# Performance work log

Hardware: AMD Instinct MI355X
Metric: run time of the kernel (lower is better)

The kernel has to match this reference:

```python
import jax, jax.numpy as jnp
import numpy as np

B, N, K = 16, 4096, 1024   # batch, mux_in, mux_out
TEMP = 2.0
COMPRESSION = 4.0


def setup_inputs() -> dict:
    key = jax.random.key(0)
    kx, kn, kl = jax.random.split(key, 3)
    x = jax.random.normal(kx, (B, N), dtype=jnp.float32)
    # Gumbel(0,1) noise, one sample per (batch, input-element), broadcast over K
    u = jax.random.uniform(kn, (B, N), dtype=jnp.float32, minval=1e-20, maxval=1.0)
    noise = -jnp.log(-jnp.log(u))
    logits = jax.random.normal(kl, (N,), dtype=jnp.float32) / COMPRESSION
    return {"x": x, "logits": logits, "noise": noise}


def reference(x, logits, noise):
    base = logits[None, :] + noise                      # [B, N] perturbed logits (same across k)
    _, topk_idx = jax.lax.top_k(base, K)                # [B, K]
    b_idx = jnp.arange(B)[:, None]

    # pos[b, i] = rank of element i in the top-k (K if not selected)
    pos = jnp.full((B, N), K, dtype=jnp.int32)
    pos = pos.at[b_idx, topk_idx].set(jnp.arange(K, dtype=jnp.int32))

    hard = jnp.zeros((B, N), dtype=base.dtype).at[b_idx, topk_idx].set(1.0)

    # Element selected at rank j is masked (-inf) for all later columns c > j.
    # Equivalent to the original scatter(-inf) -> cumsum -> re-zero sequence.
    counter = jnp.arange(K, dtype=jnp.int32)            # [K]
    masked = jnp.where(counter[None, None, :] > pos[:, :, None],
                       -jnp.inf, base[:, :, None])      # [B, N, K]

    soft = jax.nn.softmax(masked / TEMP, axis=1)        # softmax over mux_in
    collapsed = soft.sum(axis=2)                        # [B, N]

    # straight-through: hard forward, soft backward
    sample = hard - jax.lax.stop_gradient(collapsed) + collapsed
    return sample * x
```

## Files before the change

kernel.cpp:

```cpp
#include <hip/hip_runtime.h>

#define BB 16
#define NN 4096
#define KK 1024
#define THREADS 1024
#define PT (NN / THREADS)
#define NWAVES (THREADS / 64)

__device__ __forceinline__ unsigned fkey(float f) {
    unsigned u = __float_as_uint(f);
    return (u & 0x80000000u) ? ~u : (u | 0x80000000u);
}

__global__ __launch_bounds__(THREADS) void gumbel_topk_mask(
    const float* __restrict__ x,
    const float* __restrict__ logits,
    const float* __restrict__ noise,
    float* __restrict__ out)
{
    __shared__ unsigned keys[NN];
    __shared__ int wsum[NWAVES];
    __shared__ int ibcast;
    __shared__ int ecnt[THREADS];
    __shared__ int epfx[THREADS];

    const int b    = blockIdx.x;
    const int t    = threadIdx.x;
    const int lane = t & 63;
    const int wid  = t >> 6;
    const size_t row = (size_t)b * NN;

    for (int i = t; i < NN; i += THREADS)
        keys[i] = fkey(logits[i] + noise[row + i]);
    __syncthreads();

    unsigned pfx = 0u;
    for (int bit = 31; bit >= 0; --bit) {
        unsigned cand = pfx | (1u << bit);
        int cnt = 0;
        #pragma unroll
        for (int j = 0; j < PT; ++j)
            cnt += (keys[t + j * THREADS] >= cand) ? 1 : 0;
        #pragma unroll
        for (int off = 32; off > 0; off >>= 1)
            cnt += __shfl_down(cnt, off, 64);
        if (lane == 0) wsum[wid] = cnt;
        __syncthreads();
        if (t == 0) {
            int s = 0;
            for (int w = 0; w < NWAVES; ++w) s += wsum[w];
            ibcast = s;
        }
        __syncthreads();
        if (ibcast >= KK) pfx = cand;
    }
    const unsigned T = pfx;

    int packed = 0;
    #pragma unroll
    for (int j = 0; j < PT; ++j) {
        unsigned k = keys[t + j * THREADS];
        packed += (k > T) ? 1 : 0;
        packed += (k == T) ? (1 << 16) : 0;
    }
    #pragma unroll
    for (int off = 32; off > 0; off >>= 1)
        packed += __shfl_down(packed, off, 64);
    if (lane == 0) wsum[wid] = packed;
    __syncthreads();
    if (t == 0) {
        int s = 0;
        for (int w = 0; w < NWAVES; ++w) s += wsum[w];
        ibcast = s;
    }
    __syncthreads();
    const int total_g = ibcast & 0xFFFF;
    const int total_e = ibcast >> 16;
    const int rem = KK - total_g;

    const bool need_rank = (rem < total_e);
    if (need_rank) {
        int c = 0;
        for (int j = 0; j < PT; ++j)
            c += (keys[t * PT + j] == T) ? 1 : 0;
        ecnt[t] = c;
        __syncthreads();
        if (t == 0) {
            int s = 0;
            for (int i = 0; i < THREADS; ++i) { epfx[i] = s; s += ecnt[i]; }
        }
        __syncthreads();
    }

    for (int j = 0; j < PT; ++j) {
        int n = t + j * THREADS;
        unsigned k = keys[n];
        bool sel = (k > T);
        if (!sel && k == T) {
            if (!need_rank) {
                sel = true;
            } else {
                int c = n / PT;
                int r = epfx[c];
                for (int m = c * PT; m < n; ++m) r += (keys[m] == T) ? 1 : 0;
                sel = (r < rem);
            }
        }
        out[row + n] = sel ? x[row + n] : 0.0f;
    }
}

extern "C" void kernel_launch(void* const* d_in, const int* in_sizes, int n_in,
                              void* d_out, int out_size, void* d_ws, size_t ws_size,
                              hipStream_t stream) {
    const float* x      = (const float*)d_in[0];
    const float* logits = (const float*)d_in[1];
    const float* noise  = (const float*)d_in[2];
    float* out = (float*)d_out;
    (void)in_sizes; (void)n_in; (void)out_size; (void)d_ws; (void)ws_size;
    gumbel_topk_mask<<<BB, THREADS, 0, stream>>>(x, logits, noise, out);
}
```

Baseline: 25.78 us.

## Run top-k threshold search in a single wave with register keys and ballots

Replaces the 1024-thread block with one 64-lane wave per batch row, keeping 64 keys per thread in registers. The radix threshold search counts with ballot/popcount instead of shared-memory reductions and block barriers, and exits early when the count hits K exactly. Tie ranking uses a wave prefix scan, and loads and stores are vectorised. Parallelism per row drops sharply and per-thread memory accesses become strided across lanes.

```diff
diff --git a/kernel.cpp b/kernel.cpp
--- a/kernel.cpp
+++ b/kernel.cpp
@@ -3,110 +3,87 @@
 #define BB 16
 #define NN 4096
 #define KK 1024
-#define THREADS 1024
-#define PT (NN / THREADS)
-#define NWAVES (THREADS / 64)
+#define PT 64
 
 __device__ __forceinline__ unsigned fkey(float f) {
     unsigned u = __float_as_uint(f);
     return (u & 0x80000000u) ? ~u : (u | 0x80000000u);
 }
 
-__global__ __launch_bounds__(THREADS) void gumbel_topk_mask(
+__global__ __launch_bounds__(64) void gumbel_topk_mask(
     const float* __restrict__ x,
     const float* __restrict__ logits,
     const float* __restrict__ noise,
     float* __restrict__ out)
 {
-    __shared__ unsigned keys[NN];
-    __shared__ int wsum[NWAVES];
-    __shared__ int ibcast;
-    __shared__ int ecnt[THREADS];
-    __shared__ int epfx[THREADS];
+    const int b = blockIdx.x;
+    const int t = threadIdx.x;
+    const size_t row = (size_t)b * NN;
+    const int n0 = t * PT;
 
-    const int b    = blockIdx.x;
-    const int t    = threadIdx.x;
-    const int lane = t & 63;
-    const int wid  = t >> 6;
-    const size_t row = (size_t)b * NN;
-
-    for (int i = t; i < NN; i += THREADS)
-        keys[i] = fkey(logits[i] + noise[row + i]);
-    __syncthreads();
+    unsigned key[PT];
+    {
+        const float4* lg4 = (const float4*)(logits + n0);
+        const float4* nz4 = (const float4*)(noise + row + n0);
+        #pragma unroll
+        for (int q = 0; q < PT / 4; ++q) {
+            float4 l = lg4[q], z = nz4[q];
+            key[4*q+0] = fkey(l.x + z.x);
+            key[4*q+1] = fkey(l.y + z.y);
+            key[4*q+2] = fkey(l.z + z.z);
+            key[4*q+3] = fkey(l.w + z.w);
+        }
+    }
 
     unsigned pfx = 0u;
+    #pragma unroll 1
     for (int bit = 31; bit >= 0; --bit) {
-        unsigned cand = pfx | (1u << bit);
+        const unsigned cand = pfx | (1u << bit);
         int cnt = 0;
         #pragma unroll
         for (int j = 0; j < PT; ++j)
-            cnt += (keys[t + j * THREADS] >= cand) ? 1 : 0;
-        #pragma unroll
-        for (int off = 32; off > 0; off >>= 1)
-            cnt += __shfl_down(cnt, off, 64);
-        if (lane == 0) wsum[wid] = cnt;
-        __syncthreads();
-        if (t == 0) {
-            int s = 0;
-            for (int w = 0; w < NWAVES; ++w) s += wsum[w];
-            ibcast = s;
+            cnt += __popcll(__ballot(key[j] >= cand));
+        if (cnt >= KK) {
+            pfx = cand;
+            if (cnt == KK) break;
         }
-        __syncthreads();
-        if (ibcast >= KK) pfx = cand;
     }
     const unsigned T = pfx;
 
-    int packed = 0;
+    int cnt_gt = 0;
+    int ecnt   = 0;
     #pragma unroll
     for (int j = 0; j < PT; ++j) {
-        unsigned k = keys[t + j * THREADS];
-        packed += (k > T) ? 1 : 0;
-        packed += (k == T) ? (1 << 16) : 0;
+        cnt_gt += __popcll(__ballot(key[j] > T));
+        ecnt   += (key[j] == T) ? 1 : 0;
     }
+    const int rem = KK - cnt_gt;
+
+    int inc = ecnt;
     #pragma unroll
-    for (int off = 32; off > 0; off >>= 1)
-        packed += __shfl_down(packed, off, 64);
-    if (lane == 0) wsum[wid] = packed;
-    __syncthreads();
-    if (t == 0) {
-        int s = 0;
-        for (int w = 0; w < NWAVES; ++w) s += wsum[w];
-        ibcast = s;
+    for (int off = 1; off < 64; off <<= 1) {
+        int v = __shfl_up(inc, off, 64);
+        if (t >= off) inc += v;
     }
-    __syncthreads();
-    const int total_g = ibcast & 0xFFFF;
-    const int total_e = ibcast >> 16;
-    const int rem = KK - total_g;
+    int r = inc - ecnt;
 
-    const bool need_rank = (rem < total_e);
-    if (need_rank) {
-        int c = 0;
-        for (int j = 0; j < PT; ++j)
-            c += (keys[t * PT + j] == T) ? 1 : 0;
-        ecnt[t] = c;
-        __syncthreads();
-        if (t == 0) {
-            int s = 0;
-            for (int i = 0; i < THREADS; ++i) { epfx[i] = s; s += ecnt[i]; }
-        }
-        __syncthreads();
-    }
-
-    for (int j = 0; j < PT; ++j) {
-        int n = t + j * THREADS;
-        unsigned k = keys[n];
-        bool sel = (k > T);
-        if (!sel && k == T) {
-            if (!need_rank) {
-                sel = true;
-            } else {
-                int c = n / PT;
-                int r = epfx[c];
-                for (int m = c * PT; m < n; ++m) r += (keys[m] == T) ? 1 : 0;
-                sel = (r < rem);
-            }
-        }
-        out[row + n] = sel ? x[row + n] : 0.0f;
+    const float4* x4 = (const float4*)(x + row + n0);
+    float4*       o4 = (float4*)(out + row + n0);
+    #pragma unroll
+    for (int q = 0; q < PT / 4; ++q) {
+        float4 xv = x4[q];
+        unsigned k0 = key[4*q+0], k1 = key[4*q+1],
+                 k2 = key[4*q+2], k3 = key[4*q+3];
+        bool s0 = (k0 > T) || (k0 == T && (r++ < rem));
+        bool s1 = (k1 > T) || (k1 == T && (r++ < rem));
+        bool s2 = (k2 > T) || (k2 == T && (r++ < rem));
+        bool s3 = (k3 > T) || (k3 == T && (r++ < rem));
+        float4 ov;
+        ov.x = s0 ? xv.x : 0.0f;
+        ov.y = s1 ? xv.y : 0.0f;
+        ov.z = s2 ? xv.z : 0.0f;
+        ov.w = s3 ? xv.w : 0.0f;
+        o4[q] = ov;
     }
 }
 
@@ -118,5 +95,5 @@
     const float* noise  = (const float*)d_in[2];
     float* out = (float*)d_out;
     (void)in_sizes; (void)n_in; (void)out_size; (void)d_ws; (void)ws_size;
-    gumbel_topk_mask<<<BB, THREADS, 0, stream>>>(x, logits, noise, out);
+    gumbel_topk_mask<<<BB, 64, 0, stream>>>(x, logits, noise, out);
 }
```

Result: slower. 27.05 us (+4.9%).
